# Kernel tuning notes

Hardware: AMD Instinct MI355X
Metric: run time of the kernel (lower is better)

Reference implementation:

```python
import jax, jax.numpy as jnp
import numpy as np

D_MODEL = 1024
N_EXPERTS = 8
TOP_K = 2
B, S = 2, 2048


def setup_inputs() -> dict:
    key = jax.random.key(0)
    ks = jax.random.split(key, 12)
    d, e, h = D_MODEL, N_EXPERTS, 4 * D_MODEL
    sd = 1.0 / np.sqrt(d)
    sh = 1.0 / np.sqrt(h)
    return {
        "x": jax.random.normal(ks[0], (B, S, d), dtype=jnp.float32),
        "noise": jax.random.uniform(ks[1], (B, S, e), dtype=jnp.float32),
        # router linear [d, E]
        "Wr": jax.random.uniform(ks[2], (d, e), minval=-sd, maxval=sd),
        "br": jax.random.uniform(ks[3], (e,), minval=-sd, maxval=sd),
        # noise linear [d, E]
        "Wn": jax.random.uniform(ks[4], (d, e), minval=-sd, maxval=sd),
        "bn": jax.random.uniform(ks[5], (e,), minval=-sd, maxval=sd),
        # stacked expert FFN weights
        "W1": jax.random.uniform(ks[6], (e, d, h), minval=-sd, maxval=sd),
        "b1": jax.random.uniform(ks[7], (e, h), minval=-sd, maxval=sd),
        "W2": jax.random.uniform(ks[8], (e, h, d), minval=-sh, maxval=sh),
        "b2": jax.random.uniform(ks[9], (e, d), minval=-sh, maxval=sh),
    }


def _moe_forward(x, noise, Wr, br, Wn, bn, W1, b1, W2, b2):
    e = Wr.shape[-1]
    # noisy top-k router
    logits = x @ Wr + br + jax.nn.softplus(x @ Wn + bn) * noise  # [B,S,E]
    top_v, top_i = jax.lax.top_k(logits, TOP_K)                  # [B,S,K]
    # softmax over sparse top-k (non-topk entries are -inf -> weight 0)
    gates_k = jax.nn.softmax(top_v, axis=-1)                     # [B,S,K]
    gating = jnp.sum(jax.nn.one_hot(top_i, e, dtype=x.dtype) * gates_k[..., None], axis=-2)  # [B,S,E]
    # experts (dropout in eval mode = identity). Non-selected experts have
    # gate 0, so the dense weighted sum equals the masked gather/scatter.
    hdn = jax.nn.relu(jnp.einsum('bsd,edh->bseh', x, W1) + b1)   # [B,S,E,4d]
    y = jnp.einsum('bseh,ehd->bsed', hdn, W2) + b2               # [B,S,E,d]
    return jnp.einsum('bse,bsed->bsd', gating, y)


def reference(x, noise, Wr, br, Wn, bn, W1, b1, W2, b2):
    return _moe_forward(x, noise, Wr, br, Wn, bn, W1, b1, W2, b2)
```

## Files before the change

kernel.cpp:

```cpp
#include <hip/hip_runtime.h>
#include <hip/hip_bf16.h>
#include <cstdint>
#include <cstddef>

#define D_MODEL 1024
#define N_EXP   8
#define HID     4096
#define T_TOK   4096
#define NPAIR   (T_TOK * 2)

#define WS_COUNTS   0
#define WS_CURSOR   32
#define WS_OFFSETS  64
#define WS_TOKE     128
#define WS_TOKG     32896
#define WS_LTOK     65664
#define WS_LGATE    98432
#define WS_XB       131328
#define WS_WB       (WS_XB + 8388608)
#define WS_H        (WS_WB + 67108864)

typedef __attribute__((ext_vector_type(8))) short bf16x8;
typedef __attribute__((ext_vector_type(4))) float f32x4;
typedef unsigned short u16;

__device__ __forceinline__ u16 f2bf(float f) {
    unsigned u = __float_as_uint(f);
    u += 0x7FFFu + ((u >> 16) & 1u);
    return (u16)(u >> 16);
}

__device__ __forceinline__ void glds16(const void* g, void* l) {
    __builtin_amdgcn_global_load_lds(
        (const __attribute__((address_space(1))) void*)g,
        (__attribute__((address_space(3))) void*)l, 16, 0, 0);
}

__device__ __forceinline__ void chunk_map(int c, int& row, int& kc) {
    const int line = c >> 3, c8 = c & 7, u = c8 ^ (line & 7);
    row = line * 2 + (u >> 2);
    kc  = (u & 3) * 8;
}

__global__ __launch_bounds__(256) void k_router(
    const float* __restrict__ x, const float* __restrict__ noise,
    const float* __restrict__ Wr, const float* __restrict__ br,
    const float* __restrict__ Wn, const float* __restrict__ bn,
    int* __restrict__ counts, int* __restrict__ tok_e, float* __restrict__ tok_g)
{
    const int t   = blockIdx.x;
    const int tid = threadIdx.x;
    const int e   = tid & 7;
    const int g   = tid >> 3;
    const float* xr = x + (size_t)t * D_MODEL;

    float ar = 0.f, an = 0.f;
    const int ibase = g * 32;
    #pragma unroll 8
    for (int j = 0; j < 32; ++j) {
        const int i = ibase + j;
        const float xv = xr[i];
        ar = fmaf(xv, Wr[i * 8 + e], ar);
        an = fmaf(xv, Wn[i * 8 + e], an);
    }

    __shared__ float sR[256], sN[256];
    sR[tid] = ar; sN[tid] = an;
    __syncthreads();
    for (int off = 128; off >= 8; off >>= 1) {
        if (tid < off) { sR[tid] += sR[tid + off]; sN[tid] += sN[tid + off]; }
        __syncthreads();
    }

    __shared__ float lg[8];
    if (tid < 8) {
        const float z  = sN[tid] + bn[tid];
        const float sp = fmaxf(z, 0.f) + log1pf(expf(-fabsf(z)));
        lg[tid] = sR[tid] + br[tid] + sp * noise[t * 8 + tid];
    }
    __syncthreads();

    if (tid == 0) {
        float v0 = -INFINITY, v1 = -INFINITY;
        int   i0 = 0,         i1 = 0;
        #pragma unroll
        for (int ee = 0; ee < 8; ++ee) {
            const float v = lg[ee];
            if (v > v0)      { v1 = v0; i1 = i0; v0 = v; i0 = ee; }
            else if (v > v1) { v1 = v;  i1 = ee; }
        }
        const float ew  = expf(v1 - v0);
        const float inv = 1.f / (1.f + ew);
        tok_e[t * 2 + 0] = i0;
        tok_e[t * 2 + 1] = i1;
        tok_g[t * 2 + 0] = inv;
        tok_g[t * 2 + 1] = ew * inv;
        atomicAdd(&counts[i0], 1);
        atomicAdd(&counts[i1], 1);
    }
}

__global__ void k_prefix(const int* __restrict__ counts, int* __restrict__ offsets)
{
    if (threadIdx.x == 0 && blockIdx.x == 0) {
        int acc = 0;
        #pragma unroll
        for (int e = 0; e < N_EXP; ++e) { offsets[e] = acc; acc += counts[e]; }
    }
}

__global__ __launch_bounds__(256) void k_scatter(
    const int* __restrict__ tok_e, const float* __restrict__ tok_g,
    const int* __restrict__ offsets, int* __restrict__ cursor,
    int* __restrict__ list_tok, float* __restrict__ list_gate)
{
    const int gid = blockIdx.x * 256 + threadIdx.x;
    if (gid >= NPAIR) return;
    const int e = tok_e[gid];
    const int p = atomicAdd(&cursor[e], 1);
    const int slot = offsets[e] + p;
    list_tok[slot]  = gid >> 1;
    list_gate[slot] = tok_g[gid];
}

__global__ __launch_bounds__(256) void k_cvt_x(
    const float* __restrict__ in, u16* __restrict__ outp)
{
    const int i = (blockIdx.x * 256 + threadIdx.x) * 4;
    const float4 v = *(const float4*)(in + i);
    ushort4 o;
    o.x = f2bf(v.x); o.y = f2bf(v.y); o.z = f2bf(v.z); o.w = f2bf(v.w);
    *(ushort4*)(outp + i) = o;
}

__global__ __launch_bounds__(256) void k_cvtT(
    const float* __restrict__ in, u16* __restrict__ outp, int R, int C)
{
    const size_t esz = (size_t)R * C;
    const float* ine = in + (size_t)blockIdx.z * esz;
    u16* oute = outp + (size_t)blockIdx.z * esz;
    const int c0 = blockIdx.x * 32, r0 = blockIdx.y * 32;

    __shared__ float s[32][36];
    const int tid = threadIdx.x;
    const int lr = tid >> 3, lc = (tid & 7) * 4;
    const float4 v = *(const float4*)(ine + (size_t)(r0 + lr) * C + c0 + lc);
    s[lr][lc + 0] = v.x; s[lr][lc + 1] = v.y; s[lr][lc + 2] = v.z; s[lr][lc + 3] = v.w;
    __syncthreads();
    const int oc = tid >> 3, orp = (tid & 7) * 4;
    ushort4 o;
    o.x = f2bf(s[orp + 0][oc]); o.y = f2bf(s[orp + 1][oc]);
    o.z = f2bf(s[orp + 2][oc]); o.w = f2bf(s[orp + 3][oc]);
    *(ushort4*)(oute + (size_t)(c0 + oc) * R + r0 + orp) = o;
}

__global__ __launch_bounds__(256, 2) void k_ffn1(
    const u16* __restrict__ xb,
    const u16* __restrict__ W1t,
    const float* __restrict__ b1,
    const int* __restrict__ counts, const int* __restrict__ offsets,
    const int* __restrict__ list_tok,
    u16* __restrict__ H)
{
    const int bid = blockIdx.x;
    const int e   = bid >> 11;
    const int r   = bid & 2047;
    const int wg  = ((r & 7) << 8) + (r >> 3);
    const int n_t = wg >> 6;
    const int m_t = wg & 63;

    const int cnt = counts[e];
    const int m0  = m_t * 128;
    if (m0 >= cnt) return;
    const int base = offsets[e];
    const int n0   = n_t * 128;
    const u16* __restrict__ Be = W1t + (size_t)e * (HID * D_MODEL);

    __shared__ __align__(16) u16 SA[3 * 4096];
    __shared__ __align__(16) u16 SB[3 * 4096];
    __shared__ int stok[128];

    const int tid = threadIdx.x;
    if (tid < 128) stok[tid] = list_tok[base + min(m0 + tid, cnt - 1)];
    __syncthreads();

    int ar0, ak0, ar1, ak1;
    chunk_map(tid, ar0, ak0);
    chunk_map(tid + 256, ar1, ak1);
    const u16* Asrc0 = xb + (size_t)stok[ar0] * D_MODEL + ak0;
    const u16* Asrc1 = xb + (size_t)stok[ar1] * D_MODEL + ak1;
    const u16* Bsrc0 = Be + (size_t)(n0 + ar0) * D_MODEL + ak0;
    const u16* Bsrc1 = Be + (size_t)(n0 + ar1) * D_MODEL + ak1;

    const int lane = tid & 63, lr = lane & 15, hk = lane >> 4;
    const int w = tid >> 6, wm = w >> 1, wn = w & 1;
    const int colb  = ((((lr & 1) << 2) + hk) ^ (lr >> 1)) << 4;
    const int baseA = ((wm * 32 + (lr >> 1)) << 7) + colb;
    const int baseB = ((wn * 32 + (lr >> 1)) << 7) + colb;

    float bias[4];
    #pragma unroll
    for (int j = 0; j < 4; ++j) bias[j] = b1[(size_t)e * HID + n0 + wn * 64 + j * 16 + lr];

    f32x4 acc[4][4] = {};

    auto STAGE = [&](int s, int t) {
        const int kt = t * 32;
        char* Ab = (char*)SA + s * 8192;
        char* Bb = (char*)SB + s * 8192;
        glds16(Asrc0 + kt, Ab + tid * 16);
        glds16(Asrc1 + kt, Ab + (tid + 256) * 16);
        glds16(Bsrc0 + kt, Bb + tid * 16);
        glds16(Bsrc1 + kt, Bb + (tid + 256) * 16);
    };
    auto COMPUTE = [&](int s) {
        const char* Ab = (const char*)SA + s * 8192;
        const char* Bb = (const char*)SB + s * 8192;
        bf16x8 a[4], b[4];
        #pragma unroll
        for (int i = 0; i < 4; ++i) a[i] = *(const bf16x8*)(Ab + baseA + i * 1024);
        #pragma unroll
        for (int j = 0; j < 4; ++j) b[j] = *(const bf16x8*)(Bb + baseB + j * 1024);
        #pragma unroll
        for (int i = 0; i < 4; ++i)
            #pragma unroll
            for (int j = 0; j < 4; ++j)
                acc[i][j] = __builtin_amdgcn_mfma_f32_16x16x32_bf16(a[i], b[j], acc[i][j], 0, 0, 0);
    };

    const int NT = D_MODEL / 32;
    STAGE(0, 0);
    STAGE(1, 1);
    int sc = 0;
    for (int t = 0; t < NT; ++t) {
        if (t == NT - 1) { asm volatile("s_waitcnt vmcnt(0)" ::: "memory"); }
        else             { asm volatile("s_waitcnt vmcnt(4)" ::: "memory"); }
        __builtin_amdgcn_s_barrier();
        __builtin_amdgcn_sched_barrier(0);
        if (t + 2 < NT) { int ss = sc + 2; if (ss >= 3) ss -= 3; STAGE(ss, t + 2); }
        __builtin_amdgcn_sched_barrier(0);
        COMPUTE(sc);
        if (++sc == 3) sc = 0;
    }

    #pragma unroll
    for (int i = 0; i < 4; ++i) {
        #pragma unroll
        for (int g = 0; g < 4; ++g) {
            const int m = m0 + wm * 64 + i * 16 + hk * 4 + g;
            if (m < cnt) {
                u16* dst = H + (size_t)(base + m) * HID + n0 + wn * 64 + lr;
                #pragma unroll
                for (int j = 0; j < 4; ++j)
                    dst[j * 16] = f2bf(fmaxf(acc[i][j][g] + bias[j], 0.f));
            }
        }
    }
}

__global__ __launch_bounds__(256, 2) void k_ffn2(
    const u16* __restrict__ Hb,
    const u16* __restrict__ W2t,
    const float* __restrict__ b2,
    const int* __restrict__ counts, const int* __restrict__ offsets,
    const int* __restrict__ list_tok, const float* __restrict__ list_gate,
    float* __restrict__ out)
{
    const int bid = blockIdx.x;
    const int e   = bid >> 9;
    const int r   = bid & 511;
    const int wg  = ((r & 7) << 6) + (r >> 3);
    const int n_t = wg >> 6;
    const int m_t = wg & 63;

    const int cnt = counts[e];
    const int m0  = m_t * 128;
    if (m0 >= cnt) return;
    const int base = offsets[e];
    const int n0   = n_t * 128;
    const u16* __restrict__ Be = W2t + (size_t)e * (D_MODEL * HID);

    __shared__ __align__(16) u16 SA[3 * 4096];
    __shared__ __align__(16) u16 SB[3 * 4096];
    __shared__ int   s_tok[128];
    __shared__ float s_gate[128];

    const int tid = threadIdx.x;
    if (tid < 128) {
        const int sl = base + min(m0 + tid, cnt - 1);
        s_tok[tid]  = list_tok[sl];
        s_gate[tid] = list_gate[sl];
    }
    __syncthreads();

    int ar0, ak0, ar1, ak1;
    chunk_map(tid, ar0, ak0);
    chunk_map(tid + 256, ar1, ak1);
    const u16* Asrc0 = Hb + (size_t)(base + min(m0 + ar0, cnt - 1)) * HID + ak0;
    const u16* Asrc1 = Hb + (size_t)(base + min(m0 + ar1, cnt - 1)) * HID + ak1;
    const u16* Bsrc0 = Be + (size_t)(n0 + ar0) * HID + ak0;
    const u16* Bsrc1 = Be + (size_t)(n0 + ar1) * HID + ak1;

    const int lane = tid & 63, lr = lane & 15, hk = lane >> 4;
    const int w = tid >> 6, wm = w >> 1, wn = w & 1;
    const int colb  = ((((lr & 1) << 2) + hk) ^ (lr >> 1)) << 4;
    const int baseA = ((wm * 32 + (lr >> 1)) << 7) + colb;
    const int baseB = ((wn * 32 + (lr >> 1)) << 7) + colb;

    float bias[4];
    #pragma unroll
    for (int j = 0; j < 4; ++j) bias[j] = b2[(size_t)e * D_MODEL + n0 + wn * 64 + j * 16 + lr];

    f32x4 acc[4][4] = {};

    auto STAGE = [&](int s, int t) {
        const int kt = t * 32;
        char* Ab = (char*)SA + s * 8192;
        char* Bb = (char*)SB + s * 8192;
        glds16(Asrc0 + kt, Ab + tid * 16);
        glds16(Asrc1 + kt, Ab + (tid + 256) * 16);
        glds16(Bsrc0 + kt, Bb + tid * 16);
        glds16(Bsrc1 + kt, Bb + (tid + 256) * 16);
    };
    auto COMPUTE = [&](int s) {
        const char* Ab = (const char*)SA + s * 8192;
        const char* Bb = (const char*)SB + s * 8192;
        bf16x8 a[4], b[4];
        #pragma unroll
        for (int i = 0; i < 4; ++i) a[i] = *(const bf16x8*)(Ab + baseA + i * 1024);
        #pragma unroll
        for (int j = 0; j < 4; ++j) b[j] = *(const bf16x8*)(Bb + baseB + j * 1024);
        #pragma unroll
        for (int i = 0; i < 4; ++i)
            #pragma unroll
            for (int j = 0; j < 4; ++j)
                acc[i][j] = __builtin_amdgcn_mfma_f32_16x16x32_bf16(a[i], b[j], acc[i][j], 0, 0, 0);
    };

    const int NT = HID / 32;
    STAGE(0, 0);
    STAGE(1, 1);
    int sc = 0;
    for (int t = 0; t < NT; ++t) {
        if (t == NT - 1) { asm volatile("s_waitcnt vmcnt(0)" ::: "memory"); }
        else             { asm volatile("s_waitcnt vmcnt(4)" ::: "memory"); }
        __builtin_amdgcn_s_barrier();
        __builtin_amdgcn_sched_barrier(0);
        if (t + 2 < NT) { int ss = sc + 2; if (ss >= 3) ss -= 3; STAGE(ss, t + 2); }
        __builtin_amdgcn_sched_barrier(0);
        COMPUTE(sc);
        if (++sc == 3) sc = 0;
    }

    #pragma unroll
    for (int i = 0; i < 4; ++i) {
        #pragma unroll
        for (int g = 0; g < 4; ++g) {
            const int m = m0 + wm * 64 + i * 16 + hk * 4 + g;
            if (m < cnt) {
                const int   mm = m - m0;
                const int   tk = s_tok[mm];
                const float gt = s_gate[mm];
                float* dst = out + (size_t)tk * D_MODEL + n0 + wn * 64 + lr;
                #pragma unroll
                for (int j = 0; j < 4; ++j)
                    unsafeAtomicAdd(dst + j * 16, gt * (acc[i][j][g] + bias[j]));
            }
        }
    }
}

extern "C" void kernel_launch(void* const* d_in, const int* in_sizes, int n_in,
                              void* d_out, int out_size, void* d_ws, size_t ws_size,
                              hipStream_t stream)
{
    const float* x     = (const float*)d_in[0];
    const float* noise = (const float*)d_in[1];
    const float* Wr    = (const float*)d_in[2];
    const float* br    = (const float*)d_in[3];
    const float* Wn    = (const float*)d_in[4];
    const float* bn    = (const float*)d_in[5];
    const float* W1    = (const float*)d_in[6];
    const float* b1    = (const float*)d_in[7];
    const float* W2    = (const float*)d_in[8];
    const float* b2    = (const float*)d_in[9];
    float* out = (float*)d_out;

    char* ws = (char*)d_ws;
    int*   counts    = (int*)(ws + WS_COUNTS);
    int*   cursor    = (int*)(ws + WS_CURSOR);
    int*   offsets   = (int*)(ws + WS_OFFSETS);
    int*   tok_e     = (int*)(ws + WS_TOKE);
    float* tok_g     = (float*)(ws + WS_TOKG);
    int*   list_tok  = (int*)(ws + WS_LTOK);
    float* list_gate = (float*)(ws + WS_LGATE);
    u16*   xb        = (u16*)(ws + WS_XB);
    u16*   Wb        = (u16*)(ws + WS_WB);
    u16*   Hb        = (u16*)(ws + WS_H);

    hipMemsetAsync(ws, 0, 128, stream);
    hipMemsetAsync(d_out, 0, (size_t)out_size * sizeof(float), stream);

    k_cvt_x<<<T_TOK * D_MODEL / 1024, 256, 0, stream>>>(x, xb);
    k_cvtT<<<dim3(HID / 32, D_MODEL / 32, N_EXP), 256, 0, stream>>>(W1, Wb, D_MODEL, HID);
    k_router<<<T_TOK, 256, 0, stream>>>(x, noise, Wr, br, Wn, bn, counts, tok_e, tok_g);
    k_prefix<<<1, 64, 0, stream>>>(counts, offsets);
    k_scatter<<<NPAIR / 256, 256, 0, stream>>>(tok_e, tok_g, offsets, cursor,
                                               list_tok, list_gate);

    k_ffn1<<<N_EXP * 32 * 64, 256, 0, stream>>>(xb, Wb, b1, counts, offsets,
                                                list_tok, Hb);

    k_cvtT<<<dim3(D_MODEL / 32, HID / 32, N_EXP), 256, 0, stream>>>(W2, Wb, HID, D_MODEL);
    k_ffn2<<<N_EXP * 8 * 64, 256, 0, stream>>>(Hb, Wb, b2, counts, offsets,
                                               list_tok, list_gate, out);
}
```

Before: 466.6 us.

## Fuse x conversion into router, enlarge FFN1 tiles, split-K FFN2 with deeper pipeline

Folds the fp32-to-bf16 conversion of x into the router kernel and removes the separate conversion launch. FFN1 moves to 256x256 tiles with 512 threads and 8x4 MFMA accumulators per wave, which raises reuse of each shared-memory load. FFN2 splits the K dimension into two halves accumulated atomically, giving more blocks per expert, and deepens its LDS pipeline to four stages. The costs are more register pressure and lower occupancy in FFN1, and twice the atomic output traffic in FFN2.

```diff
diff --git a/kernel.cpp b/kernel.cpp
--- a/kernel.cpp
+++ b/kernel.cpp
@@ -46,13 +46,21 @@
     const float* __restrict__ x, const float* __restrict__ noise,
     const float* __restrict__ Wr, const float* __restrict__ br,
     const float* __restrict__ Wn, const float* __restrict__ bn,
-    int* __restrict__ counts, int* __restrict__ tok_e, float* __restrict__ tok_g)
+    int* __restrict__ counts, int* __restrict__ tok_e, float* __restrict__ tok_g,
+    u16* __restrict__ xb)
 {
     const int t   = blockIdx.x;
     const int tid = threadIdx.x;
     const int e   = tid & 7;
     const int g   = tid >> 3;
     const float* xr = x + (size_t)t * D_MODEL;
+
+    {
+        const float4 v4 = *(const float4*)(xr + tid * 4);
+        ushort4 o;
+        o.x = f2bf(v4.x); o.y = f2bf(v4.y); o.z = f2bf(v4.z); o.w = f2bf(v4.w);
+        *(ushort4*)(xb + (size_t)t * D_MODEL + tid * 4) = o;
+    }
 
     float ar = 0.f, an = 0.f;
     const int ibase = g * 32;
@@ -123,16 +131,6 @@
     list_gate[slot] = tok_g[gid];
 }
 
-__global__ __launch_bounds__(256) void k_cvt_x(
-    const float* __restrict__ in, u16* __restrict__ outp)
-{
-    const int i = (blockIdx.x * 256 + threadIdx.x) * 4;
-    const float4 v = *(const float4*)(in + i);
-    ushort4 o;
-    o.x = f2bf(v.x); o.y = f2bf(v.y); o.z = f2bf(v.z); o.w = f2bf(v.w);
-    *(ushort4*)(outp + i) = o;
-}
-
 __global__ __launch_bounds__(256) void k_cvtT(
     const float* __restrict__ in, u16* __restrict__ outp, int R, int C)
 {
@@ -154,7 +152,7 @@
     *(ushort4*)(oute + (size_t)(c0 + oc) * R + r0 + orp) = o;
 }
 
-__global__ __launch_bounds__(256, 2) void k_ffn1(
+__global__ __launch_bounds__(512, 1) void k_ffn1(
     const u16* __restrict__ xb,
     const u16* __restrict__ W1t,
     const float* __restrict__ b1,
@@ -163,34 +161,146 @@
     u16* __restrict__ H)
 {
     const int bid = blockIdx.x;
-    const int e   = bid >> 11;
-    const int r   = bid & 2047;
-    const int wg  = ((r & 7) << 8) + (r >> 3);
-    const int n_t = wg >> 6;
-    const int m_t = wg & 63;
+    const int e   = bid >> 9;
+    const int r   = bid & 511;
+    const int wg  = ((r & 7) << 6) + (r >> 3);
+    const int n_t = wg >> 5;
+    const int m_t = wg & 31;
+
+    const int cnt = counts[e];
+    const int m0  = m_t * 256;
+    if (m0 >= cnt) return;
+    const int base = offsets[e];
+    const int n0   = n_t * 256;
+    const u16* __restrict__ Be = W1t + (size_t)e * (HID * D_MODEL);
+
+    __shared__ __align__(16) u16 SA[3 * 8192];
+    __shared__ __align__(16) u16 SB[3 * 8192];
+    __shared__ int stok[256];
+
+    const int tid = threadIdx.x;
+    if (tid < 256) stok[tid] = list_tok[base + min(m0 + tid, cnt - 1)];
+    __syncthreads();
+
+    int ar0, ak0, ar1, ak1;
+    chunk_map(tid, ar0, ak0);
+    chunk_map(tid + 512, ar1, ak1);
+    const u16* Asrc0 = xb + (size_t)stok[ar0] * D_MODEL + ak0;
+    const u16* Asrc1 = xb + (size_t)stok[ar1] * D_MODEL + ak1;
+    const u16* Bsrc0 = Be + (size_t)(n0 + ar0) * D_MODEL + ak0;
+    const u16* Bsrc1 = Be + (size_t)(n0 + ar1) * D_MODEL + ak1;
+
+    const int lane = tid & 63, lr = lane & 15, hk = lane >> 4;
+    const int w = tid >> 6, wm = w >> 2, wn = w & 3;
+    const int colb  = ((((lr & 1) << 2) + hk) ^ (lr >> 1)) << 4;
+    const int baseA = ((wm * 64 + (lr >> 1)) << 7) + colb;
+    const int baseB = ((wn * 32 + (lr >> 1)) << 7) + colb;
+
+    float bias[4];
+    #pragma unroll
+    for (int j = 0; j < 4; ++j) bias[j] = b1[(size_t)e * HID + n0 + wn * 64 + j * 16 + lr];
+
+    f32x4 acc[8][4] = {};
+
+    auto STAGE = [&](int s, int t) {
+        const int kt = t * 32;
+        char* Ab = (char*)SA + s * 16384;
+        char* Bb = (char*)SB + s * 16384;
+        glds16(Asrc0 + kt, Ab + tid * 16);
+        glds16(Asrc1 + kt, Ab + (tid + 512) * 16);
+        glds16(Bsrc0 + kt, Bb + tid * 16);
+        glds16(Bsrc1 + kt, Bb + (tid + 512) * 16);
+    };
+    auto COMPUTE = [&](int s) {
+        const char* Ab = (const char*)SA + s * 16384;
+        const char* Bb = (const char*)SB + s * 16384;
+        bf16x8 a[8], b[4];
+        #pragma unroll
+        for (int i = 0; i < 8; ++i) a[i] = *(const bf16x8*)(Ab + baseA + i * 1024);
+        #pragma unroll
+        for (int j = 0; j < 4; ++j) b[j] = *(const bf16x8*)(Bb + baseB + j * 1024);
+        #pragma unroll
+        for (int i = 0; i < 8; ++i)
+            #pragma unroll
+            for (int j = 0; j < 4; ++j)
+                acc[i][j] = __builtin_amdgcn_mfma_f32_16x16x32_bf16(a[i], b[j], acc[i][j], 0, 0, 0);
+    };
+
+    const int NT = D_MODEL / 32;
+    STAGE(0, 0);
+    STAGE(1, 1);
+    int sc = 0;
+    for (int t = 0; t < NT; ++t) {
+        if (t == NT - 1) { asm volatile("s_waitcnt vmcnt(0)" ::: "memory"); }
+        else             { asm volatile("s_waitcnt vmcnt(4)" ::: "memory"); }
+        __builtin_amdgcn_s_barrier();
+        __builtin_amdgcn_sched_barrier(0);
+        if (t + 2 < NT) { int ss = sc + 2; if (ss >= 3) ss -= 3; STAGE(ss, t + 2); }
+        __builtin_amdgcn_sched_barrier(0);
+        COMPUTE(sc);
+        if (++sc == 3) sc = 0;
+    }
+
+    #pragma unroll
+    for (int i = 0; i < 8; ++i) {
+        #pragma unroll
+        for (int g = 0; g < 4; ++g) {
+            const int m = m0 + wm * 128 + i * 16 + hk * 4 + g;
+            if (m < cnt) {
+                u16* dst = H + (size_t)(base + m) * HID + n0 + wn * 64 + lr;
+                #pragma unroll
+                for (int j = 0; j < 4; ++j)
+                    dst[j * 16] = f2bf(fmaxf(acc[i][j][g] + bias[j], 0.f));
+            }
+        }
+    }
+}
+
+__global__ __launch_bounds__(256, 2) void k_ffn2(
+    const u16* __restrict__ Hb,
+    const u16* __restrict__ W2t,
+    const float* __restrict__ b2,
+    const int* __restrict__ counts, const int* __restrict__ offsets,
+    const int* __restrict__ list_tok, const float* __restrict__ list_gate,
+    float* __restrict__ out)
+{
+    const int bid = blockIdx.x;
+    const int e   = bid >> 10;
+    const int r   = bid & 1023;
+    const int wg  = ((r & 7) << 7) + (r >> 3);
+    const int n_t = wg >> 7;
+    const int rem = wg & 127;
+    const int m_t = rem >> 1;
+    const int kh  = rem & 1;
 
     const int cnt = counts[e];
     const int m0  = m_t * 128;
     if (m0 >= cnt) return;
     const int base = offsets[e];
     const int n0   = n_t * 128;
-    const u16* __restrict__ Be = W1t + (size_t)e * (HID * D_MODEL);
-
-    __shared__ __align__(16) u16 SA[3 * 4096];
-    __shared__ __align__(16) u16 SB[3 * 4096];
-    __shared__ int stok[128];
+    const u16* __restrict__ Be = W2t + (size_t)e * (D_MODEL * HID);
+
+    __shared__ __align__(16) u16 SA[4 * 4096];
+    __shared__ __align__(16) u16 SB[4 * 4096];
+    __shared__ int   s_tok[128];
+    __shared__ float s_gate[128];
 
     const int tid = threadIdx.x;
-    if (tid < 128) stok[tid] = list_tok[base + min(m0 + tid, cnt - 1)];
+    if (tid < 128) {
+        const int sl = base + min(m0 + tid, cnt - 1);
+        s_tok[tid]  = list_tok[sl];
+        s_gate[tid] = list_gate[sl];
+    }
     __syncthreads();
 
     int ar0, ak0, ar1, ak1;
     chunk_map(tid, ar0, ak0);
     chunk_map(tid + 256, ar1, ak1);
-    const u16* Asrc0 = xb + (size_t)stok[ar0] * D_MODEL + ak0;
-    const u16* Asrc1 = xb + (size_t)stok[ar1] * D_MODEL + ak1;
-    const u16* Bsrc0 = Be + (size_t)(n0 + ar0) * D_MODEL + ak0;
-    const u16* Bsrc1 = Be + (size_t)(n0 + ar1) * D_MODEL + ak1;
+    const int k0 = kh * (HID / 2);
+    const u16* Asrc0 = Hb + (size_t)(base + min(m0 + ar0, cnt - 1)) * HID + k0 + ak0;
+    const u16* Asrc1 = Hb + (size_t)(base + min(m0 + ar1, cnt - 1)) * HID + k0 + ak1;
+    const u16* Bsrc0 = Be + (size_t)(n0 + ar0) * HID + k0 + ak0;
+    const u16* Bsrc1 = Be + (size_t)(n0 + ar1) * HID + k0 + ak1;
 
     const int lane = tid & 63, lr = lane & 15, hk = lane >> 4;
     const int w = tid >> 6, wm = w >> 1, wn = w & 1;
@@ -200,7 +310,8 @@
 
     float bias[4];
     #pragma unroll
-    for (int j = 0; j < 4; ++j) bias[j] = b1[(size_t)e * HID + n0 + wn * 64 + j * 16 + lr];
+    for (int j = 0; j < 4; ++j)
+        bias[j] = (kh == 0) ? b2[(size_t)e * D_MODEL + n0 + wn * 64 + j * 16 + lr] : 0.f;
 
     f32x4 acc[4][4] = {};
 
@@ -228,128 +339,21 @@
                 acc[i][j] = __builtin_amdgcn_mfma_f32_16x16x32_bf16(a[i], b[j], acc[i][j], 0, 0, 0);
     };
 
-    const int NT = D_MODEL / 32;
+    const int NT = (HID / 2) / 32;
     STAGE(0, 0);
     STAGE(1, 1);
+    STAGE(2, 2);
     int sc = 0;
     for (int t = 0; t < NT; ++t) {
-        if (t == NT - 1) { asm volatile("s_waitcnt vmcnt(0)" ::: "memory"); }
-        else             { asm volatile("s_waitcnt vmcnt(4)" ::: "memory"); }
+        if (t + 2 < NT)      { asm volatile("s_waitcnt vmcnt(8)" ::: "memory"); }
+        else if (t + 1 < NT) { asm volatile("s_waitcnt vmcnt(4)" ::: "memory"); }
+        else                 { asm volatile("s_waitcnt vmcnt(0)" ::: "memory"); }
         __builtin_amdgcn_s_barrier();
         __builtin_amdgcn_sched_barrier(0);
-        if (t + 2 < NT) { int ss = sc + 2; if (ss >= 3) ss -= 3; STAGE(ss, t + 2); }
+        if (t + 3 < NT) { STAGE((sc + 3) & 3, t + 3); }
         __builtin_amdgcn_sched_barrier(0);
         COMPUTE(sc);
-        if (++sc == 3) sc = 0;
-    }
-
-    #pragma unroll
-    for (int i = 0; i < 4; ++i) {
-        #pragma unroll
-        for (int g = 0; g < 4; ++g) {
-            const int m = m0 + wm * 64 + i * 16 + hk * 4 + g;
-            if (m < cnt) {
-                u16* dst = H + (size_t)(base + m) * HID + n0 + wn * 64 + lr;
-                #pragma unroll
-                for (int j = 0; j < 4; ++j)
-                    dst[j * 16] = f2bf(fmaxf(acc[i][j][g] + bias[j], 0.f));
-            }
-        }
-    }
-}
-
-__global__ __launch_bounds__(256, 2) void k_ffn2(
-    const u16* __restrict__ Hb,
-    const u16* __restrict__ W2t,
-    const float* __restrict__ b2,
-    const int* __restrict__ counts, const int* __restrict__ offsets,
-    const int* __restrict__ list_tok, const float* __restrict__ list_gate,
-    float* __restrict__ out)
-{
-    const int bid = blockIdx.x;
-    const int e   = bid >> 9;
-    const int r   = bid & 511;
-    const int wg  = ((r & 7) << 6) + (r >> 3);
-    const int n_t = wg >> 6;
-    const int m_t = wg & 63;
-
-    const int cnt = counts[e];
-    const int m0  = m_t * 128;
-    if (m0 >= cnt) return;
-    const int base = offsets[e];
-    const int n0   = n_t * 128;
-    const u16* __restrict__ Be = W2t + (size_t)e * (D_MODEL * HID);
-
-    __shared__ __align__(16) u16 SA[3 * 4096];
-    __shared__ __align__(16) u16 SB[3 * 4096];
-    __shared__ int   s_tok[128];
-    __shared__ float s_gate[128];
-
-    const int tid = threadIdx.x;
-    if (tid < 128) {
-        const int sl = base + min(m0 + tid, cnt - 1);
-        s_tok[tid]  = list_tok[sl];
-        s_gate[tid] = list_gate[sl];
-    }
-    __syncthreads();
-
-    int ar0, ak0, ar1, ak1;
-    chunk_map(tid, ar0, ak0);
-    chunk_map(tid + 256, ar1, ak1);
-    const u16* Asrc0 = Hb + (size_t)(base + min(m0 + ar0, cnt - 1)) * HID + ak0;
-    const u16* Asrc1 = Hb + (size_t)(base + min(m0 + ar1, cnt - 1)) * HID + ak1;
-    const u16* Bsrc0 = Be + (size_t)(n0 + ar0) * HID + ak0;
-    const u16* Bsrc1 = Be + (size_t)(n0 + ar1) * HID + ak1;
-
-    const int lane = tid & 63, lr = lane & 15, hk = lane >> 4;
-    const int w = tid >> 6, wm = w >> 1, wn = w & 1;
-    const int colb  = ((((lr & 1) << 2) + hk) ^ (lr >> 1)) << 4;
-    const int baseA = ((wm * 32 + (lr >> 1)) << 7) + colb;
-    const int baseB = ((wn * 32 + (lr >> 1)) << 7) + colb;
-
-    float bias[4];
-    #pragma unroll
-    for (int j = 0; j < 4; ++j) bias[j] = b2[(size_t)e * D_MODEL + n0 + wn * 64 + j * 16 + lr];
-
-    f32x4 acc[4][4] = {};
-
-    auto STAGE = [&](int s, int t) {
-        const int kt = t * 32;
-        char* Ab = (char*)SA + s * 8192;
-        char* Bb = (char*)SB + s * 8192;
-        glds16(Asrc0 + kt, Ab + tid * 16);
-        glds16(Asrc1 + kt, Ab + (tid + 256) * 16);
-        glds16(Bsrc0 + kt, Bb + tid * 16);
-        glds16(Bsrc1 + kt, Bb + (tid + 256) * 16);
-    };
-    auto COMPUTE = [&](int s) {
-        const char* Ab = (const char*)SA + s * 8192;
-        const char* Bb = (const char*)SB + s * 8192;
-        bf16x8 a[4], b[4];
-        #pragma unroll
-        for (int i = 0; i < 4; ++i) a[i] = *(const bf16x8*)(Ab + baseA + i * 1024);
-        #pragma unroll
-        for (int j = 0; j < 4; ++j) b[j] = *(const bf16x8*)(Bb + baseB + j * 1024);
-        #pragma unroll
-        for (int i = 0; i < 4; ++i)
-            #pragma unroll
-            for (int j = 0; j < 4; ++j)
-                acc[i][j] = __builtin_amdgcn_mfma_f32_16x16x32_bf16(a[i], b[j], acc[i][j], 0, 0, 0);
-    };
-
-    const int NT = HID / 32;
-    STAGE(0, 0);
-    STAGE(1, 1);
-    int sc = 0;
-    for (int t = 0; t < NT; ++t) {
-        if (t == NT - 1) { asm volatile("s_waitcnt vmcnt(0)" ::: "memory"); }
-        else             { asm volatile("s_waitcnt vmcnt(4)" ::: "memory"); }
-        __builtin_amdgcn_s_barrier();
-        __builtin_amdgcn_sched_barrier(0);
-        if (t + 2 < NT) { int ss = sc + 2; if (ss >= 3) ss -= 3; STAGE(ss, t + 2); }
-        __builtin_amdgcn_sched_barrier(0);
-        COMPUTE(sc);
-        if (++sc == 3) sc = 0;
+        sc = (sc + 1) & 3;
     }
 
     #pragma unroll
@@ -401,17 +405,16 @@
     hipMemsetAsync(ws, 0, 128, stream);
     hipMemsetAsync(d_out, 0, (size_t)out_size * sizeof(float), stream);
 
-    k_cvt_x<<<T_TOK * D_MODEL / 1024, 256, 0, stream>>>(x, xb);
     k_cvtT<<<dim3(HID / 32, D_MODEL / 32, N_EXP), 256, 0, stream>>>(W1, Wb, D_MODEL, HID);
-    k_router<<<T_TOK, 256, 0, stream>>>(x, noise, Wr, br, Wn, bn, counts, tok_e, tok_g);
+    k_router<<<T_TOK, 256, 0, stream>>>(x, noise, Wr, br, Wn, bn, counts, tok_e, tok_g, xb);
     k_prefix<<<1, 64, 0, stream>>>(counts, offsets);
     k_scatter<<<NPAIR / 256, 256, 0, stream>>>(tok_e, tok_g, offsets, cursor,
                                                list_tok, list_gate);
 
-    k_ffn1<<<N_EXP * 32 * 64, 256, 0, stream>>>(xb, Wb, b1, counts, offsets,
+    k_ffn1<<<N_EXP * 16 * 32, 512, 0, stream>>>(xb, Wb, b1, counts, offsets,
                                                 list_tok, Hb);
 
     k_cvtT<<<dim3(D_MODEL / 32, HID / 32, N_EXP), 256, 0, stream>>>(W2, Wb, HID, D_MODEL);
-    k_ffn2<<<N_EXP * 8 * 64, 256, 0, stream>>>(Hb, Wb, b2, counts, offsets,
-                                               list_tok, list_gate, out);
-}
+    k_ffn2<<<N_EXP * 1024, 256, 0, stream>>>(Hb, Wb, b2, counts, offsets,
+                                             list_tok, list_gate, out);
+}
```

New measurement: 512.7 us. 1.1x slower.

## Switch expert GEMMs to 32x32 MFMA, fuse x conversion into router, widen transpose

Applied to the files above, without the earlier changes.

Both expert GEMM kernels now use 32x32x16 bf16 MFMA tiles (2x2 per wave) in place of 16x16x32 tiles (4x4), which cuts LDS fragment reads per MFMA and changes the epilogue mapping. The standalone x-to-bf16 conversion kernel is folded into the router kernel, removing one launch and one extra pass over x. The weight transpose-convert kernel now does 64 rows per block, converts to bf16 before staging in LDS, and writes 16-byte vectors. The epilogue stores and atomics become per-element with a different lane layout, which may change coalescing.

```diff
diff --git a/kernel.cpp b/kernel.cpp
--- a/kernel.cpp
+++ b/kernel.cpp
@@ -20,8 +20,9 @@
 #define WS_WB       (WS_XB + 8388608)
 #define WS_H        (WS_WB + 67108864)
 
-typedef __attribute__((ext_vector_type(8))) short bf16x8;
-typedef __attribute__((ext_vector_type(4))) float f32x4;
+typedef __attribute__((ext_vector_type(8)))  short bf16x8;
+typedef __attribute__((ext_vector_type(16))) float f32x16;
+typedef __attribute__((ext_vector_type(8)))  unsigned short u16x8;
 typedef unsigned short u16;
 
 __device__ __forceinline__ u16 f2bf(float f) {
@@ -41,18 +42,31 @@
     row = line * 2 + (u >> 2);
     kc  = (u & 3) * 8;
 }
+__device__ __forceinline__ int lds_off(int row, int chunk) {
+    const int line = row >> 1;
+    const int slot = (((row & 1) << 2) + chunk) ^ (line & 7);
+    return line * 128 + slot * 16;
+}
 
 __global__ __launch_bounds__(256) void k_router(
     const float* __restrict__ x, const float* __restrict__ noise,
     const float* __restrict__ Wr, const float* __restrict__ br,
     const float* __restrict__ Wn, const float* __restrict__ bn,
-    int* __restrict__ counts, int* __restrict__ tok_e, float* __restrict__ tok_g)
+    int* __restrict__ counts, int* __restrict__ tok_e, float* __restrict__ tok_g,
+    u16* __restrict__ xb)
 {
     const int t   = blockIdx.x;
     const int tid = threadIdx.x;
     const int e   = tid & 7;
     const int g   = tid >> 3;
     const float* xr = x + (size_t)t * D_MODEL;
+
+    {
+        const float4 v4 = *(const float4*)(xr + tid * 4);
+        ushort4 o;
+        o.x = f2bf(v4.x); o.y = f2bf(v4.y); o.z = f2bf(v4.z); o.w = f2bf(v4.w);
+        *(ushort4*)(xb + (size_t)t * D_MODEL + tid * 4) = o;
+    }
 
     float ar = 0.f, an = 0.f;
     const int ibase = g * 32;
@@ -123,35 +137,32 @@
     list_gate[slot] = tok_g[gid];
 }
 
-__global__ __launch_bounds__(256) void k_cvt_x(
-    const float* __restrict__ in, u16* __restrict__ outp)
-{
-    const int i = (blockIdx.x * 256 + threadIdx.x) * 4;
-    const float4 v = *(const float4*)(in + i);
-    ushort4 o;
-    o.x = f2bf(v.x); o.y = f2bf(v.y); o.z = f2bf(v.z); o.w = f2bf(v.w);
-    *(ushort4*)(outp + i) = o;
-}
-
 __global__ __launch_bounds__(256) void k_cvtT(
     const float* __restrict__ in, u16* __restrict__ outp, int R, int C)
 {
     const size_t esz = (size_t)R * C;
     const float* ine = in + (size_t)blockIdx.z * esz;
     u16* oute = outp + (size_t)blockIdx.z * esz;
-    const int c0 = blockIdx.x * 32, r0 = blockIdx.y * 32;
-
-    __shared__ float s[32][36];
+    const int c0 = blockIdx.x * 32, r0 = blockIdx.y * 64;
+
+    __shared__ u16 s[64 * 33];
     const int tid = threadIdx.x;
     const int lr = tid >> 3, lc = (tid & 7) * 4;
-    const float4 v = *(const float4*)(ine + (size_t)(r0 + lr) * C + c0 + lc);
-    s[lr][lc + 0] = v.x; s[lr][lc + 1] = v.y; s[lr][lc + 2] = v.z; s[lr][lc + 3] = v.w;
+    #pragma unroll
+    for (int p = 0; p < 2; ++p) {
+        const int row = lr + p * 32;
+        const float4 v = *(const float4*)(ine + (size_t)(r0 + row) * C + c0 + lc);
+        s[row * 33 + lc + 0] = f2bf(v.x);
+        s[row * 33 + lc + 1] = f2bf(v.y);
+        s[row * 33 + lc + 2] = f2bf(v.z);
+        s[row * 33 + lc + 3] = f2bf(v.w);
+    }
     __syncthreads();
-    const int oc = tid >> 3, orp = (tid & 7) * 4;
-    ushort4 o;
-    o.x = f2bf(s[orp + 0][oc]); o.y = f2bf(s[orp + 1][oc]);
-    o.z = f2bf(s[orp + 2][oc]); o.w = f2bf(s[orp + 3][oc]);
-    *(ushort4*)(oute + (size_t)(c0 + oc) * R + r0 + orp) = o;
+    const int oc = tid >> 3, rr = (tid & 7) * 8;
+    u16x8 o;
+    #pragma unroll
+    for (int i = 0; i < 8; ++i) o[i] = s[(rr + i) * 33 + oc];
+    *(u16x8*)(oute + (size_t)(c0 + oc) * R + r0 + rr) = o;
 }
 
 __global__ __launch_bounds__(256, 2) void k_ffn1(
@@ -192,17 +203,24 @@
     const u16* Bsrc0 = Be + (size_t)(n0 + ar0) * D_MODEL + ak0;
     const u16* Bsrc1 = Be + (size_t)(n0 + ar1) * D_MODEL + ak1;
 
-    const int lane = tid & 63, lr = lane & 15, hk = lane >> 4;
+    const int lane = tid & 63, l31 = lane & 31, l5 = lane >> 5;
     const int w = tid >> 6, wm = w >> 1, wn = w & 1;
-    const int colb  = ((((lr & 1) << 2) + hk) ^ (lr >> 1)) << 4;
-    const int baseA = ((wm * 32 + (lr >> 1)) << 7) + colb;
-    const int baseB = ((wn * 32 + (lr >> 1)) << 7) + colb;
-
-    float bias[4];
-    #pragma unroll
-    for (int j = 0; j < 4; ++j) bias[j] = b1[(size_t)e * HID + n0 + wn * 64 + j * 16 + lr];
-
-    f32x4 acc[4][4] = {};
+
+    int offA[2][2], offB[2][2];
+    #pragma unroll
+    for (int f = 0; f < 2; ++f)
+        #pragma unroll
+        for (int ks = 0; ks < 2; ++ks) {
+            offA[f][ks] = lds_off(wm * 64 + f * 32 + l31, ks * 2 + l5);
+            offB[f][ks] = lds_off(wn * 64 + f * 32 + l31, ks * 2 + l5);
+        }
+
+    float bias2[2];
+    #pragma unroll
+    for (int f = 0; f < 2; ++f)
+        bias2[f] = b1[(size_t)e * HID + n0 + wn * 64 + f * 32 + l31];
+
+    f32x16 acc[2][2] = {};
 
     auto STAGE = [&](int s, int t) {
         const int kt = t * 32;
@@ -216,16 +234,17 @@
     auto COMPUTE = [&](int s) {
         const char* Ab = (const char*)SA + s * 8192;
         const char* Bb = (const char*)SB + s * 8192;
-        bf16x8 a[4], b[4];
-        #pragma unroll
-        for (int i = 0; i < 4; ++i) a[i] = *(const bf16x8*)(Ab + baseA + i * 1024);
-        #pragma unroll
-        for (int j = 0; j < 4; ++j) b[j] = *(const bf16x8*)(Bb + baseB + j * 1024);
-        #pragma unroll
-        for (int i = 0; i < 4; ++i)
-            #pragma unroll
-            for (int j = 0; j < 4; ++j)
-                acc[i][j] = __builtin_amdgcn_mfma_f32_16x16x32_bf16(a[i], b[j], acc[i][j], 0, 0, 0);
+        #pragma unroll
+        for (int ks = 0; ks < 2; ++ks) {
+            const bf16x8 a0 = *(const bf16x8*)(Ab + offA[0][ks]);
+            const bf16x8 a1 = *(const bf16x8*)(Ab + offA[1][ks]);
+            const bf16x8 b0 = *(const bf16x8*)(Bb + offB[0][ks]);
+            const bf16x8 b1v = *(const bf16x8*)(Bb + offB[1][ks]);
+            acc[0][0] = __builtin_amdgcn_mfma_f32_32x32x16_bf16(a0, b0,  acc[0][0], 0, 0, 0);
+            acc[0][1] = __builtin_amdgcn_mfma_f32_32x32x16_bf16(a0, b1v, acc[0][1], 0, 0, 0);
+            acc[1][0] = __builtin_amdgcn_mfma_f32_32x32x16_bf16(a1, b0,  acc[1][0], 0, 0, 0);
+            acc[1][1] = __builtin_amdgcn_mfma_f32_32x32x16_bf16(a1, b1v, acc[1][1], 0, 0, 0);
+        }
     };
 
     const int NT = D_MODEL / 32;
@@ -244,18 +263,17 @@
     }
 
     #pragma unroll
-    for (int i = 0; i < 4; ++i) {
-        #pragma unroll
-        for (int g = 0; g < 4; ++g) {
-            const int m = m0 + wm * 64 + i * 16 + hk * 4 + g;
-            if (m < cnt) {
-                u16* dst = H + (size_t)(base + m) * HID + n0 + wn * 64 + lr;
-                #pragma unroll
-                for (int j = 0; j < 4; ++j)
-                    dst[j * 16] = f2bf(fmaxf(acc[i][j][g] + bias[j], 0.f));
+    for (int fi = 0; fi < 2; ++fi)
+        #pragma unroll
+        for (int fj = 0; fj < 2; ++fj)
+            #pragma unroll
+            for (int reg = 0; reg < 16; ++reg) {
+                const int m = m0 + wm * 64 + fi * 32 + (reg & 3) + 8 * (reg >> 2) + 4 * l5;
+                if (m < cnt) {
+                    H[(size_t)(base + m) * HID + n0 + wn * 64 + fj * 32 + l31] =
+                        f2bf(fmaxf(acc[fi][fj][reg] + bias2[fj], 0.f));
+                }
             }
-        }
-    }
 }
 
 __global__ __launch_bounds__(256, 2) void k_ffn2(
@@ -301,17 +319,24 @@
     const u16* Bsrc0 = Be + (size_t)(n0 + ar0) * HID + ak0;
     const u16* Bsrc1 = Be + (size_t)(n0 + ar1) * HID + ak1;
 
-    const int lane = tid & 63, lr = lane & 15, hk = lane >> 4;
+    const int lane = tid & 63, l31 = lane & 31, l5 = lane >> 5;
     const int w = tid >> 6, wm = w >> 1, wn = w & 1;
-    const int colb  = ((((lr & 1) << 2) + hk) ^ (lr >> 1)) << 4;
-    const int baseA = ((wm * 32 + (lr >> 1)) << 7) + colb;
-    const int baseB = ((wn * 32 + (lr >> 1)) << 7) + colb;
-
-    float bias[4];
-    #pragma unroll
-    for (int j = 0; j < 4; ++j) bias[j] = b2[(size_t)e * D_MODEL + n0 + wn * 64 + j * 16 + lr];
-
-    f32x4 acc[4][4] = {};
+
+    int offA[2][2], offB[2][2];
+    #pragma unroll
+    for (int f = 0; f < 2; ++f)
+        #pragma unroll
+        for (int ks = 0; ks < 2; ++ks) {
+            offA[f][ks] = lds_off(wm * 64 + f * 32 + l31, ks * 2 + l5);
+            offB[f][ks] = lds_off(wn * 64 + f * 32 + l31, ks * 2 + l5);
+        }
+
+    float bias2[2];
+    #pragma unroll
+    for (int f = 0; f < 2; ++f)
+        bias2[f] = b2[(size_t)e * D_MODEL + n0 + wn * 64 + f * 32 + l31];
+
+    f32x16 acc[2][2] = {};
 
     auto STAGE = [&](int s, int t) {
         const int kt = t * 32;
@@ -325,16 +350,17 @@
     auto COMPUTE = [&](int s) {
         const char* Ab = (const char*)SA + s * 8192;
         const char* Bb = (const char*)SB + s * 8192;
-        bf16x8 a[4], b[4];
-        #pragma unroll
-        for (int i = 0; i < 4; ++i) a[i] = *(const bf16x8*)(Ab + baseA + i * 1024);
-        #pragma unroll
-        for (int j = 0; j < 4; ++j) b[j] = *(const bf16x8*)(Bb + baseB + j * 1024);
-        #pragma unroll
-        for (int i = 0; i < 4; ++i)
-            #pragma unroll
-            for (int j = 0; j < 4; ++j)
-                acc[i][j] = __builtin_amdgcn_mfma_f32_16x16x32_bf16(a[i], b[j], acc[i][j], 0, 0, 0);
+        #pragma unroll
+        for (int ks = 0; ks < 2; ++ks) {
+            const bf16x8 a0 = *(const bf16x8*)(Ab + offA[0][ks]);
+            const bf16x8 a1 = *(const bf16x8*)(Ab + offA[1][ks]);
+            const bf16x8 b0 = *(const bf16x8*)(Bb + offB[0][ks]);
+            const bf16x8 b1v = *(const bf16x8*)(Bb + offB[1][ks]);
+            acc[0][0] = __builtin_amdgcn_mfma_f32_32x32x16_bf16(a0, b0,  acc[0][0], 0, 0, 0);
+            acc[0][1] = __builtin_amdgcn_mfma_f32_32x32x16_bf16(a0, b1v, acc[0][1], 0, 0, 0);
+            acc[1][0] = __builtin_amdgcn_mfma_f32_32x32x16_bf16(a1, b0,  acc[1][0], 0, 0, 0);
+            acc[1][1] = __builtin_amdgcn_mfma_f32_32x32x16_bf16(a1, b1v, acc[1][1], 0, 0, 0);
+        }
     };
 
     const int NT = HID / 32;
@@ -353,21 +379,20 @@
     }
 
     #pragma unroll
-    for (int i = 0; i < 4; ++i) {
-        #pragma unroll
-        for (int g = 0; g < 4; ++g) {
-            const int m = m0 + wm * 64 + i * 16 + hk * 4 + g;
-            if (m < cnt) {
-                const int   mm = m - m0;
-                const int   tk = s_tok[mm];
-                const float gt = s_gate[mm];
-                float* dst = out + (size_t)tk * D_MODEL + n0 + wn * 64 + lr;
-                #pragma unroll
-                for (int j = 0; j < 4; ++j)
-                    unsafeAtomicAdd(dst + j * 16, gt * (acc[i][j][g] + bias[j]));
+    for (int fi = 0; fi < 2; ++fi)
+        #pragma unroll
+        for (int fj = 0; fj < 2; ++fj)
+            #pragma unroll
+            for (int reg = 0; reg < 16; ++reg) {
+                const int m = m0 + wm * 64 + fi * 32 + (reg & 3) + 8 * (reg >> 2) + 4 * l5;
+                if (m < cnt) {
+                    const int   mm = m - m0;
+                    const int   tk = s_tok[mm];
+                    const float gt = s_gate[mm];
+                    unsafeAtomicAdd(out + (size_t)tk * D_MODEL + n0 + wn * 64 + fj * 32 + l31,
+                                    gt * (acc[fi][fj][reg] + bias2[fj]));
+                }
             }
-        }
-    }
 }
 
 extern "C" void kernel_launch(void* const* d_in, const int* in_sizes, int n_in,
@@ -401,9 +426,8 @@
     hipMemsetAsync(ws, 0, 128, stream);
     hipMemsetAsync(d_out, 0, (size_t)out_size * sizeof(float), stream);
 
-    k_cvt_x<<<T_TOK * D_MODEL / 1024, 256, 0, stream>>>(x, xb);
-    k_cvtT<<<dim3(HID / 32, D_MODEL / 32, N_EXP), 256, 0, stream>>>(W1, Wb, D_MODEL, HID);
-    k_router<<<T_TOK, 256, 0, stream>>>(x, noise, Wr, br, Wn, bn, counts, tok_e, tok_g);
+    k_cvtT<<<dim3(HID / 32, D_MODEL / 64, N_EXP), 256, 0, stream>>>(W1, Wb, D_MODEL, HID);
+    k_router<<<T_TOK, 256, 0, stream>>>(x, noise, Wr, br, Wn, bn, counts, tok_e, tok_g, xb);
     k_prefix<<<1, 64, 0, stream>>>(counts, offsets);
     k_scatter<<<NPAIR / 256, 256, 0, stream>>>(tok_e, tok_g, offsets, cursor,
                                                list_tok, list_gate);
@@ -411,7 +435,7 @@
     k_ffn1<<<N_EXP * 32 * 64, 256, 0, stream>>>(xb, Wb, b1, counts, offsets,
                                                 list_tok, Hb);
 
-    k_cvtT<<<dim3(D_MODEL / 32, HID / 32, N_EXP), 256, 0, stream>>>(W2, Wb, HID, D_MODEL);
+    k_cvtT<<<dim3(D_MODEL / 32, HID / 64, N_EXP), 256, 0, stream>>>(W2, Wb, HID, D_MODEL);
     k_ffn2<<<N_EXP * 8 * 64, 256, 0, stream>>>(Hb, Wb, b2, counts, offsets,
                                                list_tok, list_gate, out);
 }
```

Measured after the change: 475.1 us. About the same (+1.8%).

## Compact FFN grids, double-buffer LDS for higher occupancy, fuse x conversion into router

Applied to the files above, without the earlier changes.

The FFN kernels now launch a compact grid of work slots mapped onto (expert, m-tile) pairs from the per-expert counts, so far fewer blocks exit immediately. The LDS pipeline drops from triple to double buffering with an extra barrier per step, and launch bounds rise to 4 blocks per CU to trade pipeline depth for occupancy. The x→bf16 conversion is folded into the router kernel, and the weight transpose kernel handles 64 rows per block, converts to bf16 before the LDS store and writes 8-wide vectors. The fixed 72-slot cap assumes the per-expert tile counts sum to 72 or fewer, which holds for 8192 pairs over 8 experts (at most 64+7 tiles).

```diff
diff --git a/kernel.cpp b/kernel.cpp
--- a/kernel.cpp
+++ b/kernel.cpp
@@ -8,6 +8,7 @@
 #define HID     4096
 #define T_TOK   4096
 #define NPAIR   (T_TOK * 2)
+#define WSLOTS  72
 
 #define WS_COUNTS   0
 #define WS_CURSOR   32
@@ -22,6 +23,7 @@
 
 typedef __attribute__((ext_vector_type(8))) short bf16x8;
 typedef __attribute__((ext_vector_type(4))) float f32x4;
+typedef __attribute__((ext_vector_type(8))) unsigned short u16x8;
 typedef unsigned short u16;
 
 __device__ __forceinline__ u16 f2bf(float f) {
@@ -42,17 +44,37 @@
     kc  = (u & 3) * 8;
 }
 
+__device__ __forceinline__ bool work_map(const int* counts, int w,
+                                         int& e, int& m_t) {
+    int tot = 0; e = -1; m_t = 0;
+    #pragma unroll
+    for (int i = 0; i < N_EXP; ++i) {
+        const int tl = (counts[i] + 127) >> 7;
+        if (e < 0 && w < tot + tl) { e = i; m_t = w - tot; }
+        tot += tl;
+    }
+    return e >= 0;
+}
+
 __global__ __launch_bounds__(256) void k_router(
     const float* __restrict__ x, const float* __restrict__ noise,
     const float* __restrict__ Wr, const float* __restrict__ br,
     const float* __restrict__ Wn, const float* __restrict__ bn,
-    int* __restrict__ counts, int* __restrict__ tok_e, float* __restrict__ tok_g)
+    int* __restrict__ counts, int* __restrict__ tok_e, float* __restrict__ tok_g,
+    u16* __restrict__ xb)
 {
     const int t   = blockIdx.x;
     const int tid = threadIdx.x;
     const int e   = tid & 7;
     const int g   = tid >> 3;
     const float* xr = x + (size_t)t * D_MODEL;
+
+    {
+        const float4 v4 = *(const float4*)(xr + tid * 4);
+        ushort4 o;
+        o.x = f2bf(v4.x); o.y = f2bf(v4.y); o.z = f2bf(v4.z); o.w = f2bf(v4.w);
+        *(ushort4*)(xb + (size_t)t * D_MODEL + tid * 4) = o;
+    }
 
     float ar = 0.f, an = 0.f;
     const int ibase = g * 32;
@@ -123,38 +145,35 @@
     list_gate[slot] = tok_g[gid];
 }
 
-__global__ __launch_bounds__(256) void k_cvt_x(
-    const float* __restrict__ in, u16* __restrict__ outp)
-{
-    const int i = (blockIdx.x * 256 + threadIdx.x) * 4;
-    const float4 v = *(const float4*)(in + i);
-    ushort4 o;
-    o.x = f2bf(v.x); o.y = f2bf(v.y); o.z = f2bf(v.z); o.w = f2bf(v.w);
-    *(ushort4*)(outp + i) = o;
-}
-
 __global__ __launch_bounds__(256) void k_cvtT(
     const float* __restrict__ in, u16* __restrict__ outp, int R, int C)
 {
     const size_t esz = (size_t)R * C;
     const float* ine = in + (size_t)blockIdx.z * esz;
     u16* oute = outp + (size_t)blockIdx.z * esz;
-    const int c0 = blockIdx.x * 32, r0 = blockIdx.y * 32;
-
-    __shared__ float s[32][36];
+    const int c0 = blockIdx.x * 32, r0 = blockIdx.y * 64;
+
+    __shared__ u16 s[64 * 33];
     const int tid = threadIdx.x;
     const int lr = tid >> 3, lc = (tid & 7) * 4;
-    const float4 v = *(const float4*)(ine + (size_t)(r0 + lr) * C + c0 + lc);
-    s[lr][lc + 0] = v.x; s[lr][lc + 1] = v.y; s[lr][lc + 2] = v.z; s[lr][lc + 3] = v.w;
+    #pragma unroll
+    for (int p = 0; p < 2; ++p) {
+        const int row = lr + p * 32;
+        const float4 v = *(const float4*)(ine + (size_t)(r0 + row) * C + c0 + lc);
+        s[row * 33 + lc + 0] = f2bf(v.x);
+        s[row * 33 + lc + 1] = f2bf(v.y);
+        s[row * 33 + lc + 2] = f2bf(v.z);
+        s[row * 33 + lc + 3] = f2bf(v.w);
+    }
     __syncthreads();
-    const int oc = tid >> 3, orp = (tid & 7) * 4;
-    ushort4 o;
-    o.x = f2bf(s[orp + 0][oc]); o.y = f2bf(s[orp + 1][oc]);
-    o.z = f2bf(s[orp + 2][oc]); o.w = f2bf(s[orp + 3][oc]);
-    *(ushort4*)(oute + (size_t)(c0 + oc) * R + r0 + orp) = o;
-}
-
-__global__ __launch_bounds__(256, 2) void k_ffn1(
+    const int oc = tid >> 3, rr = (tid & 7) * 8;
+    u16x8 o;
+    #pragma unroll
+    for (int i = 0; i < 8; ++i) o[i] = s[(rr + i) * 33 + oc];
+    *(u16x8*)(oute + (size_t)(c0 + oc) * R + r0 + rr) = o;
+}
+
+__global__ __launch_bounds__(256, 4) void k_ffn1(
     const u16* __restrict__ xb,
     const u16* __restrict__ W1t,
     const float* __restrict__ b1,
@@ -163,21 +182,19 @@
     u16* __restrict__ H)
 {
     const int bid = blockIdx.x;
-    const int e   = bid >> 11;
-    const int r   = bid & 2047;
-    const int wg  = ((r & 7) << 8) + (r >> 3);
-    const int n_t = wg >> 6;
-    const int m_t = wg & 63;
-
-    const int cnt = counts[e];
-    const int m0  = m_t * 128;
-    if (m0 >= cnt) return;
+    const int n_t = (bid & 7) | (((bid >> 3) & 3) << 3);
+    const int wsl = bid >> 5;
+
+    int e, m_t;
+    if (!work_map(counts, wsl, e, m_t)) return;
+    const int cnt  = counts[e];
     const int base = offsets[e];
+    const int m0   = m_t * 128;
     const int n0   = n_t * 128;
     const u16* __restrict__ Be = W1t + (size_t)e * (HID * D_MODEL);
 
-    __shared__ __align__(16) u16 SA[3 * 4096];
-    __shared__ __align__(16) u16 SB[3 * 4096];
+    __shared__ __align__(16) u16 SA[2 * 4096];
+    __shared__ __align__(16) u16 SB[2 * 4096];
     __shared__ int stok[128];
 
     const int tid = threadIdx.x;
@@ -231,16 +248,15 @@
     const int NT = D_MODEL / 32;
     STAGE(0, 0);
     STAGE(1, 1);
-    int sc = 0;
     for (int t = 0; t < NT; ++t) {
-        if (t == NT - 1) { asm volatile("s_waitcnt vmcnt(0)" ::: "memory"); }
-        else             { asm volatile("s_waitcnt vmcnt(4)" ::: "memory"); }
+        if (t < NT - 1) { asm volatile("s_waitcnt vmcnt(4)" ::: "memory"); }
+        else            { asm volatile("s_waitcnt vmcnt(0)" ::: "memory"); }
         __builtin_amdgcn_s_barrier();
         __builtin_amdgcn_sched_barrier(0);
-        if (t + 2 < NT) { int ss = sc + 2; if (ss >= 3) ss -= 3; STAGE(ss, t + 2); }
+        COMPUTE(t & 1);
         __builtin_amdgcn_sched_barrier(0);
-        COMPUTE(sc);
-        if (++sc == 3) sc = 0;
+        __builtin_amdgcn_s_barrier();
+        if (t + 2 < NT) STAGE(t & 1, t + 2);
     }
 
     #pragma unroll
@@ -258,7 +274,7 @@
     }
 }
 
-__global__ __launch_bounds__(256, 2) void k_ffn2(
+__global__ __launch_bounds__(256, 4) void k_ffn2(
     const u16* __restrict__ Hb,
     const u16* __restrict__ W2t,
     const float* __restrict__ b2,
@@ -267,21 +283,19 @@
     float* __restrict__ out)
 {
     const int bid = blockIdx.x;
-    const int e   = bid >> 9;
-    const int r   = bid & 511;
-    const int wg  = ((r & 7) << 6) + (r >> 3);
-    const int n_t = wg >> 6;
-    const int m_t = wg & 63;
-
-    const int cnt = counts[e];
-    const int m0  = m_t * 128;
-    if (m0 >= cnt) return;
+    const int n_t = bid & 7;
+    const int wsl = bid >> 3;
+
+    int e, m_t;
+    if (!work_map(counts, wsl, e, m_t)) return;
+    const int cnt  = counts[e];
     const int base = offsets[e];
+    const int m0   = m_t * 128;
     const int n0   = n_t * 128;
     const u16* __restrict__ Be = W2t + (size_t)e * (D_MODEL * HID);
 
-    __shared__ __align__(16) u16 SA[3 * 4096];
-    __shared__ __align__(16) u16 SB[3 * 4096];
+    __shared__ __align__(16) u16 SA[2 * 4096];
+    __shared__ __align__(16) u16 SB[2 * 4096];
     __shared__ int   s_tok[128];
     __shared__ float s_gate[128];
 
@@ -340,16 +354,15 @@
     const int NT = HID / 32;
     STAGE(0, 0);
     STAGE(1, 1);
-    int sc = 0;
     for (int t = 0; t < NT; ++t) {
-        if (t == NT - 1) { asm volatile("s_waitcnt vmcnt(0)" ::: "memory"); }
-        else             { asm volatile("s_waitcnt vmcnt(4)" ::: "memory"); }
+        if (t < NT - 1) { asm volatile("s_waitcnt vmcnt(4)" ::: "memory"); }
+        else            { asm volatile("s_waitcnt vmcnt(0)" ::: "memory"); }
         __builtin_amdgcn_s_barrier();
         __builtin_amdgcn_sched_barrier(0);
-        if (t + 2 < NT) { int ss = sc + 2; if (ss >= 3) ss -= 3; STAGE(ss, t + 2); }
+        COMPUTE(t & 1);
         __builtin_amdgcn_sched_barrier(0);
-        COMPUTE(sc);
-        if (++sc == 3) sc = 0;
+        __builtin_amdgcn_s_barrier();
+        if (t + 2 < NT) STAGE(t & 1, t + 2);
     }
 
     #pragma unroll
@@ -401,17 +414,16 @@
     hipMemsetAsync(ws, 0, 128, stream);
     hipMemsetAsync(d_out, 0, (size_t)out_size * sizeof(float), stream);
 
-    k_cvt_x<<<T_TOK * D_MODEL / 1024, 256, 0, stream>>>(x, xb);
-    k_cvtT<<<dim3(HID / 32, D_MODEL / 32, N_EXP), 256, 0, stream>>>(W1, Wb, D_MODEL, HID);
-    k_router<<<T_TOK, 256, 0, stream>>>(x, noise, Wr, br, Wn, bn, counts, tok_e, tok_g);
+    k_cvtT<<<dim3(HID / 32, D_MODEL / 64, N_EXP), 256, 0, stream>>>(W1, Wb, D_MODEL, HID);
+    k_router<<<T_TOK, 256, 0, stream>>>(x, noise, Wr, br, Wn, bn, counts, tok_e, tok_g, xb);
     k_prefix<<<1, 64, 0, stream>>>(counts, offsets);
     k_scatter<<<NPAIR / 256, 256, 0, stream>>>(tok_e, tok_g, offsets, cursor,
                                                list_tok, list_gate);
 
-    k_ffn1<<<N_EXP * 32 * 64, 256, 0, stream>>>(xb, Wb, b1, counts, offsets,
-                                                list_tok, Hb);
-
-    k_cvtT<<<dim3(D_MODEL / 32, HID / 32, N_EXP), 256, 0, stream>>>(W2, Wb, HID, D_MODEL);
-    k_ffn2<<<N_EXP * 8 * 64, 256, 0, stream>>>(Hb, Wb, b2, counts, offsets,
-                                               list_tok, list_gate, out);
-}
+    k_ffn1<<<32 * WSLOTS, 256, 0, stream>>>(xb, Wb, b1, counts, offsets,
+                                            list_tok, Hb);
+
+    k_cvtT<<<dim3(D_MODEL / 32, HID / 64, N_EXP), 256, 0, stream>>>(W2, Wb, HID, D_MODEL);
+    k_ffn2<<<8 * WSLOTS, 256, 0, stream>>>(Hb, Wb, b2, counts, offsets,
+                                           list_tok, list_gate, out);
+}
```

After: 453.9 us. -2.7%, faster.
